# Kernel optimization log

Measured on AMD Instinct MI355X. Metric: run time of the kernel, lower is better.

Reference implementation:

```python
import jax, jax.numpy as jnp
import numpy as np

N, IN_DIM, OUT_DIM = 100000, 256, 256
EPS = 1e-6

def setup_inputs() -> dict:
    key = jax.random.key(0)
    ks = jax.random.split(key, 7)
    s = 1.0 / np.sqrt(IN_DIM)
    x = jax.random.normal(ks[0], (N, IN_DIM), dtype=jnp.float32)
    Wq = jax.random.uniform(ks[1], (IN_DIM, OUT_DIM), jnp.float32, -s, s)
    bq = jax.random.uniform(ks[2], (OUT_DIM,), jnp.float32, -s, s)
    Wk = jax.random.uniform(ks[3], (IN_DIM, OUT_DIM), jnp.float32, -s, s)
    bk = jax.random.uniform(ks[4], (OUT_DIM,), jnp.float32, -s, s)
    Wv = jax.random.uniform(ks[5], (IN_DIM, OUT_DIM), jnp.float32, -s, s)
    bv = jax.random.uniform(ks[6], (OUT_DIM,), jnp.float32, -s, s)
    return {"x": x, "Wq": Wq, "bq": bq, "Wk": Wk, "bk": bk, "Wv": Wv, "bv": bv}

def reference(x, Wq, bq, Wk, bk, Wv, bv):
    Q = jax.nn.relu(x @ Wq + bq)          # [N, d]
    K = jax.nn.relu(x @ Wk + bk)          # [N, d]
    V = x @ Wv + bv                       # [N, d]
    KV = jnp.einsum('nd,ne->de', K, V)    # [d, d]
    out = Q @ KV                          # [N, d]
    normalizer = Q @ K.sum(axis=0)[:, None].reshape(-1) [..., None] if False else (Q @ K.sum(axis=0)[:, None]) + EPS  # [N, 1]
    return out / normalizer
```

## Files before the change

### kernel.cpp

```cpp
#include <hip/hip_runtime.h>

typedef unsigned short u16;
typedef float f32x4 __attribute__((ext_vector_type(4)));
typedef short s16x8 __attribute__((ext_vector_type(8)));
typedef unsigned short u16x4 __attribute__((ext_vector_type(4)));

#define EPS 1e-6f

static __device__ __forceinline__ u16 f2bf(float f) {
  unsigned u = __float_as_uint(f);
  u += 0x7fffu + ((u >> 16) & 1u);
  return (u16)(u >> 16);
}
static __device__ __forceinline__ float bf2f(u16 h) {
  return __uint_as_float(((unsigned)h) << 16);
}

__global__ void wtrans_kernel(const float* __restrict__ Wq, const float* __restrict__ Wk,
                              const float* __restrict__ Wv,
                              u16* __restrict__ WqT, u16* __restrict__ WkT, u16* __restrict__ WvT) {
  int b = blockIdx.x;
  int mat = b >> 4, cg = b & 15;
  const float* W = mat == 0 ? Wq : (mat == 1 ? Wk : Wv);
  u16* WT = mat == 0 ? WqT : (mat == 1 ? WkT : WvT);
  int t = threadIdx.x;
  int c = cg * 16 + (t & 15);
  int k0 = (t >> 4) * 16;
  for (int i = 0; i < 16; ++i) {
    int k = k0 + i;
    WT[(c * 256 + k) ^ ((c & 7) << 3)] = f2bf(W[k * 256 + c]);
  }
}

__global__ __launch_bounds__(512, 2)
void qkv_kernel(const float* __restrict__ x,
                const u16* __restrict__ WqT, const u16* __restrict__ WkT, const u16* __restrict__ WvT,
                const float* __restrict__ bq, const float* __restrict__ bk, const float* __restrict__ bv,
                u16* __restrict__ Qb, u16* __restrict__ Kt, u16* __restrict__ Vt,
                float* __restrict__ ksum, int N, int NPAD) {
  __shared__ u16 xs[128][264];
  __shared__ u16 wsh[128 * 256];
  const int tid = threadIdx.x;
  const int n0 = blockIdx.x * 128;

  s16x8 w[8];
  {
    const u16* p = WqT + tid * 8;
#pragma unroll
    for (int f = 0; f < 8; ++f) w[f] = *(const s16x8*)(p + f * 4096);
  }

#pragma unroll
  for (int i = 0; i < 16; ++i) {
    int l = tid + i * 512;
    int row = l >> 6;
    int c4 = (l & 63) << 2;
    int n = n0 + row;
    float4 v = make_float4(0.f, 0.f, 0.f, 0.f);
    if (n < N) v = *(const float4*)(x + (size_t)n * 256 + c4);
    u16x4 pk;
    pk[0] = f2bf(v.x); pk[1] = f2bf(v.y); pk[2] = f2bf(v.z); pk[3] = f2bf(v.w);
    *(u16x4*)&xs[row][c4] = pk;
  }

  const int lane = tid & 63, wave = tid >> 6;
  const int quad = lane >> 4, l16 = lane & 15;
  const int wr = (wave & 1) * 64;
  const int clb = (wave >> 1) * 32;

  f32x4 accP[4][2];
  int matP = 0, colBP = 0;

  auto epilogue = [&](int matE, int colBE, f32x4 (&ac)[4][2]) {
    if (matE == 0) {
#pragma unroll
      for (int fc = 0; fc < 2; ++fc) {
        int colg4 = colBE + clb + fc * 16 + quad * 4;
        float4 bb = *(const float4*)(bq + colg4);
#pragma unroll
        for (int fr = 0; fr < 4; ++fr) {
          int n = n0 + wr + fr * 16 + l16;
          u16x4 pk;
          pk[0] = f2bf(fmaxf(ac[fr][fc][0] + bb.x, 0.f));
          pk[1] = f2bf(fmaxf(ac[fr][fc][1] + bb.y, 0.f));
          pk[2] = f2bf(fmaxf(ac[fr][fc][2] + bb.z, 0.f));
          pk[3] = f2bf(fmaxf(ac[fr][fc][3] + bb.w, 0.f));
          if (n >= N) { pk[0] = 0; pk[1] = 0; pk[2] = 0; pk[3] = 0; }
          *(u16x4*)&Qb[(size_t)n * 256 + colg4] = pk;
        }
      }
    } else {
      u16* T = (matE == 1) ? Kt : Vt;
      const float* bias = (matE == 1) ? bk : bv;
      float ksacc[2] = {0.f, 0.f};
#pragma unroll
      for (int fc = 0; fc < 2; ++fc) {
        int colg = colBE + clb + fc * 16 + l16;
        float bb = bias[colg];
#pragma unroll
        for (int fr = 0; fr < 4; ++fr) {
          int n = n0 + wr + fr * 16 + quad * 4;
          u16x4 pk;
#pragma unroll
          for (int j = 0; j < 4; ++j) {
            float v = ac[fr][fc][j] + bb;
            if (matE == 1) v = fmaxf(v, 0.f);
            bool ok = (n + j < N);
            pk[j] = ok ? f2bf(v) : (u16)0;
            if (matE == 1) ksacc[fc] += ok ? v : 0.f;
          }
          *(u16x4*)&T[(size_t)colg * NPAD + n] = pk;
        }
      }
      if (matE == 1) {
#pragma unroll
        for (int fc = 0; fc < 2; ++fc) {
          float v = ksacc[fc];
          v += __shfl_xor(v, 16);
          v += __shfl_xor(v, 32);
          if (quad == 0) atomicAdd(&ksum[colBE + clb + fc * 16 + l16], v);
        }
      }
    }
  };

  for (int ph = 0; ph < 6; ++ph) {
    const int mat = ph >> 1, colB = (ph & 1) * 128;

    __syncthreads();
#pragma unroll
    for (int f = 0; f < 8; ++f) *(s16x8*)&wsh[f * 4096 + tid * 8] = w[f];
    __syncthreads();

    if (ph + 1 < 6) {
      int matn = (ph + 1) >> 1, colBn = ((ph + 1) & 1) * 128;
      const u16* WTn = matn == 0 ? WqT : (matn == 1 ? WkT : WvT);
      const u16* p = WTn + colBn * 256 + tid * 8;
#pragma unroll
      for (int f = 0; f < 8; ++f) w[f] = *(const s16x8*)(p + f * 4096);
    }

    if (ph > 0) epilogue(matP, colBP, accP);

    f32x4 acc[4][2] = {};
#pragma unroll
    for (int c = 0; c < 8; ++c) {
      const int kc = c * 32;
      s16x8 a[4], b[2];
#pragma unroll
      for (int f = 0; f < 4; ++f) a[f] = *(const s16x8*)&xs[wr + f * 16 + l16][kc + quad * 8];
#pragma unroll
      for (int f = 0; f < 2; ++f) {
        int cl = clb + f * 16 + l16;
        b[f] = *(const s16x8*)&wsh[(cl * 256 + kc + quad * 8) ^ ((cl & 7) << 3)];
      }
      if (mat == 0) {
#pragma unroll
        for (int fr = 0; fr < 4; ++fr)
#pragma unroll
          for (int fc = 0; fc < 2; ++fc)
            acc[fr][fc] = __builtin_amdgcn_mfma_f32_16x16x32_bf16(b[fc], a[fr], acc[fr][fc], 0, 0, 0);
      } else {
#pragma unroll
        for (int fr = 0; fr < 4; ++fr)
#pragma unroll
          for (int fc = 0; fc < 2; ++fc)
            acc[fr][fc] = __builtin_amdgcn_mfma_f32_16x16x32_bf16(a[fr], b[fc], acc[fr][fc], 0, 0, 0);
      }
    }
#pragma unroll
    for (int fr = 0; fr < 4; ++fr)
#pragma unroll
      for (int fc = 0; fc < 2; ++fc) accP[fr][fc] = acc[fr][fc];
    matP = mat; colBP = colB;
  }
  epilogue(matP, colBP, accP);
}

__global__ __launch_bounds__(256, 3)
void kv_kernel(const u16* __restrict__ Kt, const u16* __restrict__ Vt,
               float* __restrict__ P, int NPAD, int S) {
  const int tid = threadIdx.x;
  const int s = blockIdx.x % S;
  const int g = blockIdx.x / S;
  const int ti = (g >> 1) * 128;
  const int tj = (g & 1) * 128;
  const int lane = tid & 63, wave = tid >> 6;
  const int quad = lane >> 4, l16 = lane & 15;
  const int we = (wave >> 1) * 64;
  const int wd = (wave & 1) * 64;
  const int NC64 = NPAD >> 6;

  const u16* ap = Vt + (size_t)(ti + we + l16) * NPAD + quad * 8;
  const u16* bp = Kt + (size_t)(tj + wd + l16) * NPAD + quad * 8;

  f32x4 acc[4][4] = {};
  for (int c = s; c < NC64; c += S) {
    size_t nb = (size_t)c << 6;
    s16x8 a0[4], a1[4], b0[4], b1[4];
#pragma unroll
    for (int f = 0; f < 4; ++f) {
      const u16* ar = ap + (size_t)f * 16 * NPAD + nb;
      const u16* br = bp + (size_t)f * 16 * NPAD + nb;
      a0[f] = *(const s16x8*)ar; a1[f] = *(const s16x8*)(ar + 32);
      b0[f] = *(const s16x8*)br; b1[f] = *(const s16x8*)(br + 32);
    }
#pragma unroll
    for (int fr = 0; fr < 4; ++fr)
#pragma unroll
      for (int fc = 0; fc < 4; ++fc)
        acc[fr][fc] = __builtin_amdgcn_mfma_f32_16x16x32_bf16(a0[fr], b0[fc], acc[fr][fc], 0, 0, 0);
#pragma unroll
    for (int fr = 0; fr < 4; ++fr)
#pragma unroll
      for (int fc = 0; fc < 4; ++fc)
        acc[fr][fc] = __builtin_amdgcn_mfma_f32_16x16x32_bf16(a1[fr], b1[fc], acc[fr][fc], 0, 0, 0);
  }

  float* Pp = P + (size_t)s * 65536;
#pragma unroll
  for (int fr = 0; fr < 4; ++fr)
#pragma unroll
    for (int fc = 0; fc < 4; ++fc) {
      int d = tj + wd + fc * 16 + l16;
      int e0 = ti + we + fr * 16 + quad * 4;
      *(f32x4*)&Pp[(size_t)d * 256 + e0] = acc[fr][fc];
    }
}

__global__ void kvred_kernel(const float* __restrict__ P, u16* __restrict__ KVtb, int nsp) {
  int d = blockIdx.x;
  int e = threadIdx.x;
  float s = 0.f;
  for (int sp = 0; sp < nsp; ++sp) s += P[(size_t)sp * 65536 + d * 256 + e];
  KVtb[e * 256 + d] = f2bf(s);
}

__global__ __launch_bounds__(256, 4)
void out_kernel(const u16* __restrict__ Qb, const u16* __restrict__ KVtb,
                const float* __restrict__ ksum, float* __restrict__ out,
                int N, int NPAD) {
  __shared__ u16 Qs[64][264];
  __shared__ float ks[256];
  __shared__ float nrmp[256];
  __shared__ float nrm[64];
  const int tid = threadIdx.x;
  const int r0 = blockIdx.x * 64;

#pragma unroll
  for (int i = 0; i < 8; ++i) {
    int l = tid + i * 256;
    int row = l >> 5;
    int seg = (l & 31) << 3;
    *(s16x8*)&Qs[row][seg] = *(const s16x8*)&Qb[(size_t)(r0 + row) * 256 + seg];
  }
  ks[tid] = ksum[tid];
  __syncthreads();

  {
    int r = tid & 63, h = tid >> 6;
    float sa = 0.f;
#pragma unroll
    for (int dd = 0; dd < 64; dd += 8) {
      int d = h * 64 + dd;
      s16x8 q = *(const s16x8*)&Qs[r][d];
#pragma unroll
      for (int j = 0; j < 8; ++j) sa += bf2f((u16)q[j]) * ks[d + j];
    }
    nrmp[tid] = sa;
  }
  __syncthreads();
  if (tid < 64)
    nrm[tid] = nrmp[tid] + nrmp[tid + 64] + nrmp[tid + 128] + nrmp[tid + 192] + EPS;
  __syncthreads();

  const int lane = tid & 63, wave = tid >> 6;
  const int quad = lane >> 4, l16 = lane & 15;
  const int eg = wave * 64;

  const u16* ap = KVtb + (size_t)(eg + l16) * 256 + quad * 8;

  f32x4 acc[4][4] = {};
#pragma unroll 2
  for (int c = 0; c < 8; ++c) {
    int kc = c * 32;
    s16x8 a[4], b[4];
#pragma unroll
    for (int f = 0; f < 4; ++f) a[f] = *(const s16x8*)(ap + f * 16 * 256 + kc);
#pragma unroll
    for (int f = 0; f < 4; ++f) b[f] = *(const s16x8*)&Qs[f * 16 + l16][kc + quad * 8];
#pragma unroll
    for (int fr = 0; fr < 4; ++fr)
#pragma unroll
      for (int fc = 0; fc < 4; ++fc)
        acc[fr][fc] = __builtin_amdgcn_mfma_f32_16x16x32_bf16(a[fr], b[fc], acc[fr][fc], 0, 0, 0);
  }

#pragma unroll
  for (int fc = 0; fc < 4; ++fc) {
    int rl = fc * 16 + l16;
    int rg = r0 + rl;
    float inv = 1.0f / nrm[rl];
    if (rg < N) {
#pragma unroll
      for (int fr = 0; fr < 4; ++fr) {
        int e0 = eg + fr * 16 + quad * 4;
        f32x4 o;
        o[0] = acc[fr][fc][0] * inv;
        o[1] = acc[fr][fc][1] * inv;
        o[2] = acc[fr][fc][2] * inv;
        o[3] = acc[fr][fc][3] * inv;
        *(f32x4*)&out[(size_t)rg * 256 + e0] = o;
      }
    }
  }
}

extern "C" void kernel_launch(void* const* d_in, const int* in_sizes, int n_in,
                              void* d_out, int out_size, void* d_ws, size_t ws_size,
                              hipStream_t stream) {
  const float* x  = (const float*)d_in[0];
  const float* Wq = (const float*)d_in[1];
  const float* bq = (const float*)d_in[2];
  const float* Wk = (const float*)d_in[3];
  const float* bk = (const float*)d_in[4];
  const float* Wv = (const float*)d_in[5];
  const float* bv = (const float*)d_in[6];
  float* out = (float*)d_out;

  int N = in_sizes[0] / 256;
  int NPAD = ((N + 127) / 128) * 128;
  int nblkQ = NPAD / 128;
  int nblkO = NPAD / 64;

  size_t szT = (size_t)256 * NPAD * sizeof(u16);
  size_t fixed = 3 * szT + (size_t)65536 * sizeof(u16) + 256 * sizeof(float)
               + 3 * (size_t)65536 * sizeof(u16);
  int S = 128;
  if (fixed + (size_t)S * 65536 * sizeof(float) > ws_size) S = 64;
  if (fixed + (size_t)S * 65536 * sizeof(float) > ws_size) S = 32;

  char* p = (char*)d_ws;
  u16* Kt = (u16*)p; p += szT;
  u16* Vt = (u16*)p; p += szT;
  u16* Qb = (u16*)p; p += szT;
  float* P = (float*)p; p += (size_t)S * 65536 * sizeof(float);
  u16* KVtb = (u16*)p; p += (size_t)65536 * sizeof(u16);
  float* ksum = (float*)p; p += 256 * sizeof(float);
  u16* WqT = (u16*)p; p += (size_t)65536 * sizeof(u16);
  u16* WkT = (u16*)p; p += (size_t)65536 * sizeof(u16);
  u16* WvT = (u16*)p; p += (size_t)65536 * sizeof(u16);

  hipMemsetAsync(ksum, 0, 256 * sizeof(float), stream);
  wtrans_kernel<<<48, 256, 0, stream>>>(Wq, Wk, Wv, WqT, WkT, WvT);
  qkv_kernel<<<nblkQ, 512, 0, stream>>>(x, WqT, WkT, WvT, bq, bk, bv, Qb, Kt, Vt, ksum, N, NPAD);
  kv_kernel<<<S * 4, 256, 0, stream>>>(Kt, Vt, P, NPAD, S);
  kvred_kernel<<<256, 256, 0, stream>>>(P, KVtb, S);
  out_kernel<<<nblkO, 256, 0, stream>>>(Qb, KVtb, ksum, out, N, NPAD);
}
```

Measured before the change: 427.9 us.

## Stream weight K-chunks through small LDS buffer to raise QKV kernel occupancy

The QKV projection kernel no longer stages a whole 128x256 weight slice in LDS. Each of 48 iterations loads one 128x32 weight chunk into a small padded LDS tile, double-buffered in registers, and the XOR swizzle moves from the weights to the x tile. LDS use drops from about 130 KB to about 75 KB, so launch bounds rise from 2 to 4 blocks per CU for latency hiding, at the cost of two barriers per K-chunk instead of per phase and no overlap of the epilogue with the next phase. The KV split count S also starts at 256 instead of 128.

```diff
diff --git a/kernel.cpp b/kernel.cpp
--- a/kernel.cpp
+++ b/kernel.cpp
@@ -28,27 +28,20 @@
   int k0 = (t >> 4) * 16;
   for (int i = 0; i < 16; ++i) {
     int k = k0 + i;
-    WT[(c * 256 + k) ^ ((c & 7) << 3)] = f2bf(W[k * 256 + c]);
-  }
-}
-
-__global__ __launch_bounds__(512, 2)
+    WT[c * 256 + k] = f2bf(W[k * 256 + c]);
+  }
+}
+
+__global__ __launch_bounds__(512, 4)
 void qkv_kernel(const float* __restrict__ x,
                 const u16* __restrict__ WqT, const u16* __restrict__ WkT, const u16* __restrict__ WvT,
                 const float* __restrict__ bq, const float* __restrict__ bk, const float* __restrict__ bv,
                 u16* __restrict__ Qb, u16* __restrict__ Kt, u16* __restrict__ Vt,
                 float* __restrict__ ksum, int N, int NPAD) {
-  __shared__ u16 xs[128][264];
-  __shared__ u16 wsh[128 * 256];
+  __shared__ u16 xs[128 * 256];
+  __shared__ u16 wst[128 * 40];
   const int tid = threadIdx.x;
   const int n0 = blockIdx.x * 128;
-
-  s16x8 w[8];
-  {
-    const u16* p = WqT + tid * 8;
-#pragma unroll
-    for (int f = 0; f < 8; ++f) w[f] = *(const s16x8*)(p + f * 4096);
-  }
 
 #pragma unroll
   for (int i = 0; i < 16; ++i) {
@@ -60,7 +53,7 @@
     if (n < N) v = *(const float4*)(x + (size_t)n * 256 + c4);
     u16x4 pk;
     pk[0] = f2bf(v.x); pk[1] = f2bf(v.y); pk[2] = f2bf(v.z); pk[3] = f2bf(v.w);
-    *(u16x4*)&xs[row][c4] = pk;
+    *(u16x4*)&xs[row * 256 + (c4 ^ ((row & 7) << 3))] = pk;
   }
 
   const int lane = tid & 63, wave = tid >> 6;
@@ -68,113 +61,112 @@
   const int wr = (wave & 1) * 64;
   const int clb = (wave >> 1) * 32;
 
-  f32x4 accP[4][2];
-  int matP = 0, colBP = 0;
-
-  auto epilogue = [&](int matE, int colBE, f32x4 (&ac)[4][2]) {
-    if (matE == 0) {
-#pragma unroll
-      for (int fc = 0; fc < 2; ++fc) {
-        int colg4 = colBE + clb + fc * 16 + quad * 4;
-        float4 bb = *(const float4*)(bq + colg4);
-#pragma unroll
-        for (int fr = 0; fr < 4; ++fr) {
-          int n = n0 + wr + fr * 16 + l16;
-          u16x4 pk;
-          pk[0] = f2bf(fmaxf(ac[fr][fc][0] + bb.x, 0.f));
-          pk[1] = f2bf(fmaxf(ac[fr][fc][1] + bb.y, 0.f));
-          pk[2] = f2bf(fmaxf(ac[fr][fc][2] + bb.z, 0.f));
-          pk[3] = f2bf(fmaxf(ac[fr][fc][3] + bb.w, 0.f));
-          if (n >= N) { pk[0] = 0; pk[1] = 0; pk[2] = 0; pk[3] = 0; }
-          *(u16x4*)&Qb[(size_t)n * 256 + colg4] = pk;
+  const int scol = tid >> 2, sseg = (tid & 3) * 8;
+
+  auto cptr = [&](int it) -> const u16* {
+    int ph = it >> 3, kc = (it & 7) * 32;
+    int mat = ph >> 1, colB = (ph & 1) * 128;
+    const u16* WT = mat == 0 ? WqT : (mat == 1 ? WkT : WvT);
+    return WT + (size_t)(colB + scol) * 256 + kc + sseg;
+  };
+
+  s16x8 w0 = *(const s16x8*)cptr(0);
+  s16x8 w1 = *(const s16x8*)cptr(1);
+
+  f32x4 acc[4][2] = {};
+  for (int it = 0; it < 48; ++it) {
+    const int ph = it >> 3, kc = (it & 7) * 32;
+    const int mat = ph >> 1, colBase = (ph & 1) * 128;
+
+    __syncthreads();
+    *(s16x8*)&wst[scol * 40 + sseg] = (it & 1) ? w1 : w0;
+    __syncthreads();
+
+    if (it + 2 < 48) {
+      if (it & 1) w1 = *(const s16x8*)cptr(it + 2);
+      else        w0 = *(const s16x8*)cptr(it + 2);
+    }
+
+    s16x8 a[4], b[2];
+#pragma unroll
+    for (int f = 0; f < 4; ++f) {
+      int r = wr + f * 16 + l16;
+      a[f] = *(const s16x8*)&xs[r * 256 + ((kc + quad * 8) ^ ((r & 7) << 3))];
+    }
+#pragma unroll
+    for (int f = 0; f < 2; ++f) b[f] = *(const s16x8*)&wst[(clb + f * 16 + l16) * 40 + quad * 8];
+
+    if (mat == 0) {
+#pragma unroll
+      for (int fr = 0; fr < 4; ++fr)
+#pragma unroll
+        for (int fc = 0; fc < 2; ++fc)
+          acc[fr][fc] = __builtin_amdgcn_mfma_f32_16x16x32_bf16(b[fc], a[fr], acc[fr][fc], 0, 0, 0);
+    } else {
+#pragma unroll
+      for (int fr = 0; fr < 4; ++fr)
+#pragma unroll
+        for (int fc = 0; fc < 2; ++fc)
+          acc[fr][fc] = __builtin_amdgcn_mfma_f32_16x16x32_bf16(a[fr], b[fc], acc[fr][fc], 0, 0, 0);
+    }
+
+    if ((it & 7) == 7) {
+      if (mat == 0) {
+#pragma unroll
+        for (int fc = 0; fc < 2; ++fc) {
+          int colg4 = colBase + clb + fc * 16 + quad * 4;
+          float4 bb = *(const float4*)(bq + colg4);
+#pragma unroll
+          for (int fr = 0; fr < 4; ++fr) {
+            int n = n0 + wr + fr * 16 + l16;
+            u16x4 pk;
+            pk[0] = f2bf(fmaxf(acc[fr][fc][0] + bb.x, 0.f));
+            pk[1] = f2bf(fmaxf(acc[fr][fc][1] + bb.y, 0.f));
+            pk[2] = f2bf(fmaxf(acc[fr][fc][2] + bb.z, 0.f));
+            pk[3] = f2bf(fmaxf(acc[fr][fc][3] + bb.w, 0.f));
+            if (n >= N) { pk[0] = 0; pk[1] = 0; pk[2] = 0; pk[3] = 0; }
+            *(u16x4*)&Qb[(size_t)n * 256 + colg4] = pk;
+          }
+        }
+      } else {
+        u16* T = (mat == 1) ? Kt : Vt;
+        const float* bias = (mat == 1) ? bk : bv;
+        float ksacc[2] = {0.f, 0.f};
+#pragma unroll
+        for (int fc = 0; fc < 2; ++fc) {
+          int colg = colBase + clb + fc * 16 + l16;
+          float bb = bias[colg];
+#pragma unroll
+          for (int fr = 0; fr < 4; ++fr) {
+            int n = n0 + wr + fr * 16 + quad * 4;
+            u16x4 pk;
+#pragma unroll
+            for (int j = 0; j < 4; ++j) {
+              float v = acc[fr][fc][j] + bb;
+              if (mat == 1) v = fmaxf(v, 0.f);
+              bool ok = (n + j < N);
+              pk[j] = ok ? f2bf(v) : (u16)0;
+              if (mat == 1) ksacc[fc] += ok ? v : 0.f;
+            }
+            *(u16x4*)&T[(size_t)colg * NPAD + n] = pk;
+          }
+        }
+        if (mat == 1) {
+#pragma unroll
+          for (int fc = 0; fc < 2; ++fc) {
+            float v = ksacc[fc];
+            v += __shfl_xor(v, 16);
+            v += __shfl_xor(v, 32);
+            if (quad == 0) atomicAdd(&ksum[colBase + clb + fc * 16 + l16], v);
+          }
         }
       }
-    } else {
-      u16* T = (matE == 1) ? Kt : Vt;
-      const float* bias = (matE == 1) ? bk : bv;
-      float ksacc[2] = {0.f, 0.f};
-#pragma unroll
-      for (int fc = 0; fc < 2; ++fc) {
-        int colg = colBE + clb + fc * 16 + l16;
-        float bb = bias[colg];
-#pragma unroll
-        for (int fr = 0; fr < 4; ++fr) {
-          int n = n0 + wr + fr * 16 + quad * 4;
-          u16x4 pk;
-#pragma unroll
-          for (int j = 0; j < 4; ++j) {
-            float v = ac[fr][fc][j] + bb;
-            if (matE == 1) v = fmaxf(v, 0.f);
-            bool ok = (n + j < N);
-            pk[j] = ok ? f2bf(v) : (u16)0;
-            if (matE == 1) ksacc[fc] += ok ? v : 0.f;
-          }
-          *(u16x4*)&T[(size_t)colg * NPAD + n] = pk;
-        }
-      }
-      if (matE == 1) {
-#pragma unroll
-        for (int fc = 0; fc < 2; ++fc) {
-          float v = ksacc[fc];
-          v += __shfl_xor(v, 16);
-          v += __shfl_xor(v, 32);
-          if (quad == 0) atomicAdd(&ksum[colBE + clb + fc * 16 + l16], v);
-        }
-      }
-    }
-  };
-
-  for (int ph = 0; ph < 6; ++ph) {
-    const int mat = ph >> 1, colB = (ph & 1) * 128;
-
-    __syncthreads();
-#pragma unroll
-    for (int f = 0; f < 8; ++f) *(s16x8*)&wsh[f * 4096 + tid * 8] = w[f];
-    __syncthreads();
-
-    if (ph + 1 < 6) {
-      int matn = (ph + 1) >> 1, colBn = ((ph + 1) & 1) * 128;
-      const u16* WTn = matn == 0 ? WqT : (matn == 1 ? WkT : WvT);
-      const u16* p = WTn + colBn * 256 + tid * 8;
-#pragma unroll
-      for (int f = 0; f < 8; ++f) w[f] = *(const s16x8*)(p + f * 4096);
-    }
-
-    if (ph > 0) epilogue(matP, colBP, accP);
-
-    f32x4 acc[4][2] = {};
-#pragma unroll
-    for (int c = 0; c < 8; ++c) {
-      const int kc = c * 32;
-      s16x8 a[4], b[2];
-#pragma unroll
-      for (int f = 0; f < 4; ++f) a[f] = *(const s16x8*)&xs[wr + f * 16 + l16][kc + quad * 8];
-#pragma unroll
-      for (int f = 0; f < 2; ++f) {
-        int cl = clb + f * 16 + l16;
-        b[f] = *(const s16x8*)&wsh[(cl * 256 + kc + quad * 8) ^ ((cl & 7) << 3)];
-      }
-      if (mat == 0) {
-#pragma unroll
-        for (int fr = 0; fr < 4; ++fr)
-#pragma unroll
-          for (int fc = 0; fc < 2; ++fc)
-            acc[fr][fc] = __builtin_amdgcn_mfma_f32_16x16x32_bf16(b[fc], a[fr], acc[fr][fc], 0, 0, 0);
-      } else {
-#pragma unroll
-        for (int fr = 0; fr < 4; ++fr)
-#pragma unroll
-          for (int fc = 0; fc < 2; ++fc)
-            acc[fr][fc] = __builtin_amdgcn_mfma_f32_16x16x32_bf16(a[fr], b[fc], acc[fr][fc], 0, 0, 0);
-      }
-    }
-#pragma unroll
-    for (int fr = 0; fr < 4; ++fr)
-#pragma unroll
-      for (int fc = 0; fc < 2; ++fc) accP[fr][fc] = acc[fr][fc];
-    matP = mat; colBP = colB;
-  }
-  epilogue(matP, colBP, accP);
+#pragma unroll
+      for (int fr = 0; fr < 4; ++fr)
+#pragma unroll
+        for (int fc = 0; fc < 2; ++fc) acc[fr][fc] = (f32x4){0.f, 0.f, 0.f, 0.f};
+    }
+  }
 }
 
 __global__ __launch_bounds__(256, 3)
@@ -336,9 +328,8 @@
   size_t szT = (size_t)256 * NPAD * sizeof(u16);
   size_t fixed = 3 * szT + (size_t)65536 * sizeof(u16) + 256 * sizeof(float)
                + 3 * (size_t)65536 * sizeof(u16);
-  int S = 128;
-  if (fixed + (size_t)S * 65536 * sizeof(float) > ws_size) S = 64;
-  if (fixed + (size_t)S * 65536 * sizeof(float) > ws_size) S = 32;
+  int S = 256;
+  while (S > 32 && fixed + (size_t)S * 65536 * sizeof(float) > ws_size) S >>= 1;
 
   char* p = (char*)d_ws;
   u16* Kt = (u16*)p; p += szT;
```

Result: slower. 493.2 us (+15.3%).
